# Kernel tuning notes

Measured on AMD Instinct MI355X. Metric: run time of the kernel, lower is better.

## Reference

```python
import jax, jax.numpy as jnp
import numpy as np

N = 4096      # num_nodes (tokens)
D = 1024      # in_features
GC1 = 1024    # gc hidden sizes
GC2 = 1024
FC1 = 512     # fc hidden
NUM_CLASSES = 2
FW = 8        # forward band width
BW = 8        # backward band width


def setup_inputs() -> dict:
    key = jax.random.key(0)
    ks = jax.random.split(key, 6)
    s = 0.02
    return {
        "x": jax.random.normal(ks[0], (N, D), jnp.float32),
        # sequential band weights, initialized to 0.5 as in the module
        "fw_w": 0.5 * jnp.ones((FW,), jnp.float32),
        "bw_w": 0.5 * jnp.ones((BW,), jnp.float32),
        # graph-conv layer weights (linear: h @ W + b, then A @ .)
        "gc_w1": s * jax.random.normal(ks[1], (D, GC1), jnp.float32),
        "gc_b1": jnp.zeros((GC1,), jnp.float32),
        "gc_w2": s * jax.random.normal(ks[2], (GC1, GC2), jnp.float32),
        "gc_b2": jnp.zeros((GC2,), jnp.float32),
        # fully-connected head
        "fc_w1": s * jax.random.normal(ks[3], (GC2, FC1), jnp.float32),
        "fc_b1": jnp.zeros((FC1,), jnp.float32),
        "fc_w2": s * jax.random.normal(ks[4], (FC1, NUM_CLASSES), jnp.float32),
        "fc_b2": jnp.zeros((NUM_CLASSES,), jnp.float32),
    }


def build_adjacency(fw_w, bw_w, n):
    # banded adjacency: self-loops + forward superdiagonals + backward subdiagonals,
    # then symmetric normalization D^{-1/2} A D^{-1/2}
    a = jnp.eye(n, dtype=fw_w.dtype)
    for j in range(fw_w.shape[0]):          # small fixed band loop (FW)
        a = a + fw_w[j] * jnp.eye(n, k=j + 1, dtype=fw_w.dtype)
    for j in range(bw_w.shape[0]):          # small fixed band loop (BW)
        a = a + bw_w[j] * jnp.eye(n, k=-(j + 1), dtype=bw_w.dtype)
    d = a.sum(axis=1) ** -0.5               # row degrees
    return d[:, None] * a * d[None, :]


def reference(x, fw_w, bw_w, gc_w1, gc_b1, gc_w2, gc_b2, fc_w1, fc_b1, fc_w2, fc_b2):
    a = build_adjacency(fw_w, bw_w, x.shape[0])          # [N, N]
    # GC layers: selu(A @ (H W + b)); dropout=0.0 -> identity
    h = jax.nn.selu(a @ (x @ gc_w1 + gc_b1))             # [N, GC1]
    h = jax.nn.selu(a @ (h @ gc_w2 + gc_b2))             # [N, GC2]
    pooled = h.mean(axis=0)                              # mean pooling over nodes
    z = jax.nn.selu(pooled @ fc_w1 + fc_b1)              # [FC1]
    return z @ fc_w2 + fc_b2                             # [NUM_CLASSES] logits
```

## Files before the change

kernel.cpp:

```cpp
#include <hip/hip_runtime.h>
#include <stdint.h>

#define NND 4096
#define DIM 1024
#define FC1N 512

typedef __attribute__((ext_vector_type(8))) short short8;
typedef __attribute__((ext_vector_type(4))) float floatx4;
typedef unsigned short u16;
typedef unsigned int u32;

__device__ __forceinline__ u16 f2bf(float f) {
    union { float f; u32 u; } a; a.f = f;
    u32 u = a.u;
    return (u16)((u + 0x7fffu + ((u >> 16) & 1u)) >> 16);
}
__device__ __forceinline__ float bf2f(u16 h) {
    union { u32 u; float f; } a; a.u = ((u32)h) << 16; return a.f;
}
__device__ __forceinline__ float selu_f(float x) {
    const float lam = 1.0507009873554805f;
    const float alp = 1.6732632423543772f;
    return x > 0.f ? lam * x : lam * alp * (expf(x) - 1.f);
}
__device__ __forceinline__ void async16(const u16* g, u16* l) {
    __builtin_amdgcn_global_load_lds((const __attribute__((address_space(1))) u32*)g,
                                     (__attribute__((address_space(3))) u32*)l, 16, 0, 0);
}

__global__ void k_prep(const float* __restrict__ x, const float* __restrict__ w1,
                       const float* __restrict__ w2, u16* __restrict__ Xb,
                       u16* __restrict__ W1t, u16* __restrict__ W2t,
                       float* __restrict__ zero_base) {
    int b = blockIdx.x, t = threadIdx.x;
    if (b < 512) {
        const float4* xin = (const float4*)x;
        ushort4* xo = (ushort4*)Xb;
        int base = b * 2048 + t;
        #pragma unroll
        for (int i = 0; i < 8; ++i) {
            float4 v = xin[base + i * 256];
            ushort4 o; o.x = f2bf(v.x); o.y = f2bf(v.y); o.z = f2bf(v.z); o.w = f2bf(v.w);
            xo[base + i * 256] = o;
        }
        if (b == 0)
            for (int i = t; i < 1537; i += 256) zero_base[i] = 0.f;
        return;
    }
    int job = b - 512;
    const float* in = (job & 256) ? w2 : w1;
    u16* out = (job & 256) ? W2t : W1t;
    int tl = job & 255;
    int r0 = (tl >> 4) * 64, c0 = (tl & 15) * 64;
    __shared__ float tile[64][65];
    int cg = t & 15, rb = t >> 4;
    #pragma unroll
    for (int rr = 0; rr < 4; ++rr) {
        int row = rb + rr * 16;
        float4 v = *(const float4*)(in + (size_t)(r0 + row) * DIM + c0 + cg * 4);
        tile[row][cg * 4 + 0] = v.x; tile[row][cg * 4 + 1] = v.y;
        tile[row][cg * 4 + 2] = v.z; tile[row][cg * 4 + 3] = v.w;
    }
    __syncthreads();
    #pragma unroll
    for (int rr = 0; rr < 4; ++rr) {
        int nl = rb + rr * 16;
        int kl = cg * 4;
        ushort4 o;
        o.x = f2bf(tile[kl + 0][nl]); o.y = f2bf(tile[kl + 1][nl]);
        o.z = f2bf(tile[kl + 2][nl]); o.w = f2bf(tile[kl + 3][nl]);
        *(ushort4*)(out + (size_t)(c0 + nl) * DIM + r0 + kl) = o;
    }
}

__launch_bounds__(256, 4)
__global__ void k_gemmband(const u16* __restrict__ A, const u16* __restrict__ Bt,
                           const float* __restrict__ bias,
                           const float* __restrict__ fw, const float* __restrict__ bw,
                           u16* __restrict__ H, float* __restrict__ pooled, int mode) {
    __shared__ __align__(16) u16 stage[10240];
    __shared__ float sdinv_s[96];
    __shared__ float wt_s[17];
    __shared__ float pl[4][64];

    const int m0 = blockIdx.x * 64, n0 = blockIdx.y * 64;
    const int t = threadIdx.x, wave = t >> 6, lane = t & 63;
    const int q = lane >> 4, r = lane & 15;
    const int wm = wave & 1, wn = wave >> 1;
    const int Lrow = lane >> 3, Lseg = lane & 7;

    if (t < 96) {
        int g = m0 - 16 + t;
        float s = 0.f;
        if (g >= 0 && g < NND) {
            float deg = 1.f;
            #pragma unroll
            for (int j = 0; j < 8; ++j) {
                if (g + j + 1 < NND) deg += fw[j];
                if (g - j - 1 >= 0)  deg += bw[j];
            }
            s = 1.f / sqrtf(deg);
        }
        sdinv_s[t] = s;
    } else if (t >= 128 && t < 145) {
        int o = t - 136;
        wt_s[t - 128] = (o == 0) ? 1.f : (o > 0 ? fw[o - 1] : bw[-o - 1]);
    }

    floatx4 acc[3][2];
    #pragma unroll
    for (int mt = 0; mt < 3; ++mt) { acc[mt][0] = (floatx4)0.f; acc[mt][1] = (floatx4)0.f; }

    #pragma unroll 1
    for (int k = 0; k < 16; ++k) {
        int kb = k * 64;
        #pragma unroll
        for (int i = 0; i < 5; ++i) {
            int c = wave * 5 + i;
            u16* dst = &stage[c * 512];
            const u16* src;
            if (c < 12) {
                int row = c * 8 + Lrow;
                int g = m0 - 16 + row;
                g = g < 0 ? 0 : (g > NND - 1 ? NND - 1 : g);
                src = A + (size_t)g * DIM + kb + ((Lseg ^ Lrow) * 8);
            } else {
                int row = (c - 12) * 8 + Lrow;
                src = Bt + (size_t)(n0 + row) * DIM + kb + ((Lseg ^ Lrow) * 8);
            }
            async16(src, dst);
        }
        __syncthreads();
        const u16* As = &stage[0];
        const u16* Bs = &stage[6144];
        #pragma unroll
        for (int s = 0; s < 2; ++s) {
            int j0 = s * 4 + q;
            short8 bfr[2];
            #pragma unroll
            for (int nt = 0; nt < 2; ++nt) {
                int nl = wn * 32 + nt * 16 + r;
                bfr[nt] = *(const short8*)&Bs[nl * 64 + ((j0 ^ (nl & 7)) * 8)];
            }
            #pragma unroll
            for (int mt = 0; mt < 3; ++mt) {
                int ml = wm * 48 + mt * 16 + r;
                short8 afr = *(const short8*)&As[ml * 64 + ((j0 ^ (ml & 7)) * 8)];
                acc[mt][0] = __builtin_amdgcn_mfma_f32_16x16x32_bf16(afr, bfr[0], acc[mt][0], 0, 0, 0);
                acc[mt][1] = __builtin_amdgcn_mfma_f32_16x16x32_bf16(afr, bfr[1], acc[mt][1], 0, 0, 0);
            }
        }
        __syncthreads();
    }
    u16 (*Yt)[66] = (u16(*)[66])&stage[0];
    #pragma unroll
    for (int nt = 0; nt < 2; ++nt) {
        int col = wn * 32 + nt * 16 + r;
        float bv = bias[n0 + col];
        #pragma unroll
        for (int mt = 0; mt < 3; ++mt)
            #pragma unroll
            for (int rr = 0; rr < 4; ++rr)
                Yt[wm * 48 + mt * 16 + q * 4 + rr][col] = f2bf(acc[mt][nt][rr] + bv);
    }
    __syncthreads();

    int col = t & 63;
    int r0w = (t >> 6) * 16;
    float w[17];
    #pragma unroll
    for (int o = 0; o < 17; ++o) w[o] = wt_s[o];
    float win[17];
    #pragma unroll
    for (int j = 0; j < 16; ++j) {
        int T = r0w + 8 + j;
        win[j] = sdinv_s[T] * bf2f(Yt[T][col]);
    }
    float psum = 0.f;
    #pragma unroll
    for (int rr = 0; rr < 16; ++rr) {
        int T = r0w + 24 + rr;
        win[(rr + 16) % 17] = sdinv_s[T] * bf2f(Yt[T][col]);
        float a = 0.f;
        #pragma unroll
        for (int o = 0; o < 17; ++o) a += w[o] * win[(rr + o) % 17];
        float v = selu_f(a * sdinv_s[r0w + 16 + rr]);
        if (mode == 0) H[(size_t)(m0 + r0w + rr) * DIM + n0 + col] = f2bf(v);
        else psum += v;
    }
    if (mode) {
        pl[wave][col] = psum;
        __syncthreads();
        if (t < 64)
            atomicAdd(&pooled[n0 + t], pl[0][t] + pl[1][t] + pl[2][t] + pl[3][t]);
    }
}

__global__ void k_fc(const float* __restrict__ pooled, const float* __restrict__ fcw1,
                     const float* __restrict__ fcb1, const float* __restrict__ fcw2,
                     const float* __restrict__ fcb2, float* __restrict__ zacc,
                     u32* __restrict__ cnt, float* __restrict__ out) {
    __shared__ float red[1024];
    __shared__ int lastf;
    int o = threadIdx.x, b = blockIdx.x;
    int kb = b * 64;
    float s = 0.f;
    #pragma unroll 4
    for (int kk = 0; kk < 64; ++kk)
        s += pooled[kb + kk] * fcw1[(size_t)(kb + kk) * FC1N + o];
    atomicAdd(&zacc[o], s * (1.f / NND));
    __threadfence();
    __syncthreads();
    if (o == 0) lastf = (atomicAdd(cnt, 1u) == 15u);
    __syncthreads();
    if (!lastf) return;
    __threadfence();
    float zv = atomicAdd(&zacc[o], 0.f);
    float z = selu_f(zv + fcb1[o]);
    red[o] = z * fcw2[o * 2 + 0];
    red[512 + o] = z * fcw2[o * 2 + 1];
    __syncthreads();
    #pragma unroll 1
    for (int s2 = 256; s2 > 0; s2 >>= 1) {
        if (o < s2) { red[o] += red[o + s2]; red[512 + o] += red[512 + o + s2]; }
        __syncthreads();
    }
    if (o == 0) { out[0] = red[0] + fcb2[0]; out[1] = red[1] + fcb2[1]; }
}

extern "C" void kernel_launch(void* const* d_in, const int* in_sizes, int n_in,
                              void* d_out, int out_size, void* d_ws, size_t ws_size,
                              hipStream_t stream) {
    const float* x     = (const float*)d_in[0];
    const float* fw    = (const float*)d_in[1];
    const float* bw    = (const float*)d_in[2];
    const float* gc_w1 = (const float*)d_in[3];
    const float* gc_b1 = (const float*)d_in[4];
    const float* gc_w2 = (const float*)d_in[5];
    const float* gc_b2 = (const float*)d_in[6];
    const float* fc_w1 = (const float*)d_in[7];
    const float* fc_b1 = (const float*)d_in[8];
    const float* fc_w2 = (const float*)d_in[9];
    const float* fc_b2 = (const float*)d_in[10];
    float* out = (float*)d_out;

    char* ws = (char*)d_ws;
    u16*   Xb     = (u16*)(ws);
    u16*   H1     = (u16*)(ws + (8u  << 20));
    u16*   W1t    = (u16*)(ws + (16u << 20));
    u16*   W2t    = (u16*)(ws + (18u << 20));
    float* pooled = (float*)(ws + (20u << 20));
    float* zacc   = pooled + 1024;
    u32*   cnt    = (u32*)(zacc + 512);

    k_prep<<<1024, 256, 0, stream>>>(x, gc_w1, gc_w2, Xb, W1t, W2t, pooled);
    k_gemmband<<<dim3(64, 16), 256, 0, stream>>>(Xb, W1t, gc_b1, fw, bw, H1, nullptr, 0);
    k_gemmband<<<dim3(64, 16), 256, 0, stream>>>(H1, W2t, gc_b2, fw, bw, nullptr, pooled, 1);
    k_fc<<<16, 512, 0, stream>>>(pooled, fc_w1, fc_b1, fc_w2, fc_b2, zacc, cnt, out);
}
```

Measured before the change: 145.8 us.

## Apply band adjacency before GEMM and use larger double-buffered GEMM tiles

The banded normalized adjacency is now applied to the input before each linear layer (A(XW+b) = (AX)W + rowsum(A)·b). The x band is fused into the prep conversion, and a separate band kernel runs between the two GEMMs. This removes the 16-row halo recompute and the LDS transpose epilogue from the GEMM, which now uses 128x128 tiles with double-buffered async LDS loads and adds a precomputed row-sum vector for the bias term. The cost is an extra kernel launch and an extra bf16 round trip of H1 through memory, plus lower occupancy from launch bounds of 1 and larger LDS use.

```diff
diff --git a/kernel.cpp b/kernel.cpp
--- a/kernel.cpp
+++ b/kernel.cpp
@@ -27,27 +27,83 @@
     __builtin_amdgcn_global_load_lds((const __attribute__((address_space(1))) u32*)g,
                                      (__attribute__((address_space(3))) u32*)l, 16, 0, 0);
 }
+__device__ __forceinline__ float dinv_row(int i, const float* fw, const float* bw) {
+    if (i < 0 || i >= NND) return 0.f;
+    float deg = 1.f;
+    #pragma unroll
+    for (int j = 0; j < 8; ++j) {
+        if (i + j + 1 < NND) deg += fw[j];
+        if (i - j - 1 >= 0)  deg += bw[j];
+    }
+    return 1.f / sqrtf(deg);
+}
 
 __global__ void k_prep(const float* __restrict__ x, const float* __restrict__ w1,
-                       const float* __restrict__ w2, u16* __restrict__ Xb,
+                       const float* __restrict__ w2, const float* __restrict__ fw,
+                       const float* __restrict__ bw, u16* __restrict__ XA,
                        u16* __restrict__ W1t, u16* __restrict__ W2t,
-                       float* __restrict__ zero_base) {
+                       float* __restrict__ fzone) {
     int b = blockIdx.x, t = threadIdx.x;
-    if (b < 512) {
-        const float4* xin = (const float4*)x;
-        ushort4* xo = (ushort4*)Xb;
-        int base = b * 2048 + t;
-        #pragma unroll
-        for (int i = 0; i < 8; ++i) {
-            float4 v = xin[base + i * 256];
-            ushort4 o; o.x = f2bf(v.x); o.y = f2bf(v.y); o.z = f2bf(v.z); o.w = f2bf(v.w);
-            xo[base + i * 256] = o;
-        }
-        if (b == 0)
-            for (int i = t; i < 1537; i += 256) zero_base[i] = 0.f;
+    if (b < 256) {
+        __shared__ float sdv[48];
+        __shared__ float wts[17];
+        int m0 = b * 16;
+        if (t < 48) sdv[t] = dinv_row(m0 - 16 + t, fw, bw);
+        else if (t >= 64 && t < 81) {
+            int o = t - 72;
+            wts[t - 64] = (o == 0) ? 1.f : (o > 0 ? fw[o - 1] : bw[-o - 1]);
+        }
+        __syncthreads();
+        const float4* X4 = (const float4*)x;
+        ushort4* O4 = (ushort4*)XA;
+        float4 win[17];
+        #pragma unroll
+        for (int j = 0; j < 16; ++j) {
+            int g = m0 - 8 + j;
+            int gc = g < 0 ? 0 : g;
+            float s = sdv[8 + j];
+            float4 v = X4[(size_t)gc * 256 + t];
+            win[j].x = v.x * s; win[j].y = v.y * s; win[j].z = v.z * s; win[j].w = v.w * s;
+        }
+        #pragma unroll
+        for (int rr = 0; rr < 16; ++rr) {
+            int g = m0 + 8 + rr;
+            int gc = g > NND - 1 ? NND - 1 : g;
+            float s = sdv[24 + rr];
+            float4 v = X4[(size_t)gc * 256 + t];
+            int wi = (rr + 16) % 17;
+            win[wi].x = v.x * s; win[wi].y = v.y * s; win[wi].z = v.z * s; win[wi].w = v.w * s;
+            float ax = 0.f, ay = 0.f, az = 0.f, aw = 0.f;
+            #pragma unroll
+            for (int o = 0; o < 17; ++o) {
+                float w = wts[o];
+                const float4& u = win[(rr + o) % 17];
+                ax += w * u.x; ay += w * u.y; az += w * u.z; aw += w * u.w;
+            }
+            float so = sdv[16 + rr];
+            ushort4 ov;
+            ov.x = f2bf(ax * so); ov.y = f2bf(ay * so);
+            ov.z = f2bf(az * so); ov.w = f2bf(aw * so);
+            O4[(size_t)(m0 + rr) * 256 + t] = ov;
+        }
         return;
     }
-    int job = b - 512;
+    if (b == 768) {
+        float* rs = fzone + 2048;
+        for (int it = 0; it < 16; ++it) {
+            int i = it * 256 + t;
+            float di = dinv_row(i, fw, bw);
+            float s = di;
+            #pragma unroll
+            for (int kk = 1; kk <= 8; ++kk)
+                s += fw[kk - 1] * dinv_row(i + kk, fw, bw)
+                   + bw[kk - 1] * dinv_row(i - kk, fw, bw);
+            rs[i] = di * s;
+        }
+        for (int i = t; i < 1537; i += 256) fzone[i] = 0.f;
+        return;
+    }
+    int job = b - 256;
     const float* in = (job & 256) ? w2 : w1;
     u16* out = (job & 256) ? W2t : W1t;
     int tl = job & 255;
@@ -73,126 +129,150 @@
     }
 }
 
-__launch_bounds__(256, 4)
-__global__ void k_gemmband(const u16* __restrict__ A, const u16* __restrict__ Bt,
-                           const float* __restrict__ bias,
-                           const float* __restrict__ fw, const float* __restrict__ bw,
-                           u16* __restrict__ H, float* __restrict__ pooled, int mode) {
-    __shared__ __align__(16) u16 stage[10240];
-    __shared__ float sdinv_s[96];
-    __shared__ float wt_s[17];
-    __shared__ float pl[4][64];
-
-    const int m0 = blockIdx.x * 64, n0 = blockIdx.y * 64;
+__global__ void k_band(const u16* __restrict__ in, u16* __restrict__ outp,
+                       const float* __restrict__ fw, const float* __restrict__ bw) {
+    __shared__ float sdv[48];
+    __shared__ float wts[17];
+    int b = blockIdx.x, t = threadIdx.x;
+    int m0 = b * 16;
+    if (t < 48) sdv[t] = dinv_row(m0 - 16 + t, fw, bw);
+    else if (t >= 64 && t < 81) {
+        int o = t - 72;
+        wts[t - 64] = (o == 0) ? 1.f : (o > 0 ? fw[o - 1] : bw[-o - 1]);
+    }
+    __syncthreads();
+    const ushort4* I4 = (const ushort4*)in;
+    ushort4* O4 = (ushort4*)outp;
+    float4 win[17];
+    #pragma unroll
+    for (int j = 0; j < 16; ++j) {
+        int g = m0 - 8 + j;
+        int gc = g < 0 ? 0 : g;
+        float s = sdv[8 + j];
+        ushort4 v = I4[(size_t)gc * 256 + t];
+        win[j].x = bf2f(v.x) * s; win[j].y = bf2f(v.y) * s;
+        win[j].z = bf2f(v.z) * s; win[j].w = bf2f(v.w) * s;
+    }
+    #pragma unroll
+    for (int rr = 0; rr < 16; ++rr) {
+        int g = m0 + 8 + rr;
+        int gc = g > NND - 1 ? NND - 1 : g;
+        float s = sdv[24 + rr];
+        ushort4 v = I4[(size_t)gc * 256 + t];
+        int wi = (rr + 16) % 17;
+        win[wi].x = bf2f(v.x) * s; win[wi].y = bf2f(v.y) * s;
+        win[wi].z = bf2f(v.z) * s; win[wi].w = bf2f(v.w) * s;
+        float ax = 0.f, ay = 0.f, az = 0.f, aw = 0.f;
+        #pragma unroll
+        for (int o = 0; o < 17; ++o) {
+            float w = wts[o];
+            const float4& u = win[(rr + o) % 17];
+            ax += w * u.x; ay += w * u.y; az += w * u.z; aw += w * u.w;
+        }
+        float so = sdv[16 + rr];
+        ushort4 ov;
+        ov.x = f2bf(ax * so); ov.y = f2bf(ay * so);
+        ov.z = f2bf(az * so); ov.w = f2bf(aw * so);
+        O4[(size_t)(m0 + rr) * 256 + t] = ov;
+    }
+}
+
+__launch_bounds__(256, 1)
+__global__ void k_gemm(const u16* __restrict__ A, const u16* __restrict__ Bt,
+                       const float* __restrict__ bias, const float* __restrict__ rs,
+                       u16* __restrict__ H, float* __restrict__ pooled, int mode) {
+    __shared__ __align__(16) u16 stage[2][16384];
+    const int m0 = blockIdx.x * 128, n0 = blockIdx.y * 128;
     const int t = threadIdx.x, wave = t >> 6, lane = t & 63;
     const int q = lane >> 4, r = lane & 15;
     const int wm = wave & 1, wn = wave >> 1;
     const int Lrow = lane >> 3, Lseg = lane & 7;
 
-    if (t < 96) {
-        int g = m0 - 16 + t;
-        float s = 0.f;
-        if (g >= 0 && g < NND) {
-            float deg = 1.f;
-            #pragma unroll
-            for (int j = 0; j < 8; ++j) {
-                if (g + j + 1 < NND) deg += fw[j];
-                if (g - j - 1 >= 0)  deg += bw[j];
-            }
-            s = 1.f / sqrtf(deg);
-        }
-        sdinv_s[t] = s;
-    } else if (t >= 128 && t < 145) {
-        int o = t - 136;
-        wt_s[t - 128] = (o == 0) ? 1.f : (o > 0 ? fw[o - 1] : bw[-o - 1]);
-    }
-
-    floatx4 acc[3][2];
-    #pragma unroll
-    for (int mt = 0; mt < 3; ++mt) { acc[mt][0] = (floatx4)0.f; acc[mt][1] = (floatx4)0.f; }
+    floatx4 acc[4][4];
+    #pragma unroll
+    for (int i = 0; i < 4; ++i)
+        #pragma unroll
+        for (int j = 0; j < 4; ++j) acc[i][j] = (floatx4)0.f;
+
+    #pragma unroll
+    for (int i = 0; i < 8; ++i) {
+        int c = wave * 8 + i;
+        u16* dst = &stage[0][c * 512];
+        const u16* src = (c < 16)
+            ? A  + (size_t)(m0 + c * 8 + Lrow) * DIM + ((Lseg ^ Lrow) * 8)
+            : Bt + (size_t)(n0 + (c - 16) * 8 + Lrow) * DIM + ((Lseg ^ Lrow) * 8);
+        async16(src, dst);
+    }
 
     #pragma unroll 1
     for (int k = 0; k < 16; ++k) {
-        int kb = k * 64;
-        #pragma unroll
-        for (int i = 0; i < 5; ++i) {
-            int c = wave * 5 + i;
-            u16* dst = &stage[c * 512];
-            const u16* src;
-            if (c < 12) {
-                int row = c * 8 + Lrow;
-                int g = m0 - 16 + row;
-                g = g < 0 ? 0 : (g > NND - 1 ? NND - 1 : g);
-                src = A + (size_t)g * DIM + kb + ((Lseg ^ Lrow) * 8);
-            } else {
-                int row = (c - 12) * 8 + Lrow;
-                src = Bt + (size_t)(n0 + row) * DIM + kb + ((Lseg ^ Lrow) * 8);
-            }
-            async16(src, dst);
-        }
+        int cur = k & 1;
         __syncthreads();
-        const u16* As = &stage[0];
-        const u16* Bs = &stage[6144];
+        if (k < 15) {
+            int kb = (k + 1) * 64;
+            #pragma unroll
+            for (int i = 0; i < 8; ++i) {
+                int c = wave * 8 + i;
+                u16* dst = &stage[cur ^ 1][c * 512];
+                const u16* src = (c < 16)
+                    ? A  + (size_t)(m0 + c * 8 + Lrow) * DIM + kb + ((Lseg ^ Lrow) * 8)
+                    : Bt + (size_t)(n0 + (c - 16) * 8 + Lrow) * DIM + kb + ((Lseg ^ Lrow) * 8);
+                async16(src, dst);
+            }
+        }
+        const u16* As = &stage[cur][0];
+        const u16* Bs = &stage[cur][8192];
         #pragma unroll
         for (int s = 0; s < 2; ++s) {
             int j0 = s * 4 + q;
-            short8 bfr[2];
-            #pragma unroll
-            for (int nt = 0; nt < 2; ++nt) {
-                int nl = wn * 32 + nt * 16 + r;
+            short8 bfr[4];
+            #pragma unroll
+            for (int nt = 0; nt < 4; ++nt) {
+                int nl = wn * 64 + nt * 16 + r;
                 bfr[nt] = *(const short8*)&Bs[nl * 64 + ((j0 ^ (nl & 7)) * 8)];
             }
             #pragma unroll
-            for (int mt = 0; mt < 3; ++mt) {
-                int ml = wm * 48 + mt * 16 + r;
+            for (int mt = 0; mt < 4; ++mt) {
+                int ml = wm * 64 + mt * 16 + r;
                 short8 afr = *(const short8*)&As[ml * 64 + ((j0 ^ (ml & 7)) * 8)];
-                acc[mt][0] = __builtin_amdgcn_mfma_f32_16x16x32_bf16(afr, bfr[0], acc[mt][0], 0, 0, 0);
-                acc[mt][1] = __builtin_amdgcn_mfma_f32_16x16x32_bf16(afr, bfr[1], acc[mt][1], 0, 0, 0);
-            }
-        }
+                #pragma unroll
+                for (int nt = 0; nt < 4; ++nt)
+                    acc[mt][nt] = __builtin_amdgcn_mfma_f32_16x16x32_bf16(afr, bfr[nt], acc[mt][nt], 0, 0, 0);
+            }
+        }
+    }
+
+    float psum[4] = {0.f, 0.f, 0.f, 0.f};
+    float bv[4];
+    #pragma unroll
+    for (int nt = 0; nt < 4; ++nt) bv[nt] = bias[n0 + wn * 64 + nt * 16 + r];
+    #pragma unroll
+    for (int mt = 0; mt < 4; ++mt) {
+        #pragma unroll
+        for (int rr = 0; rr < 4; ++rr) {
+            int m = m0 + wm * 64 + mt * 16 + q * 4 + rr;
+            float rsm = rs[m];
+            #pragma unroll
+            for (int nt = 0; nt < 4; ++nt) {
+                float v = selu_f(acc[mt][nt][rr] + rsm * bv[nt]);
+                if (mode == 0)
+                    H[(size_t)m * DIM + n0 + wn * 64 + nt * 16 + r] = f2bf(v);
+                else psum[nt] += v;
+            }
+        }
+    }
+    if (mode) {
+        float* PL = (float*)&stage[0][0];
+        #pragma unroll
+        for (int nt = 0; nt < 4; ++nt)
+            PL[(wn * 64 + nt * 16 + r) * 8 + wm * 4 + q] = psum[nt];
         __syncthreads();
-    }
-    u16 (*Yt)[66] = (u16(*)[66])&stage[0];
-    #pragma unroll
-    for (int nt = 0; nt < 2; ++nt) {
-        int col = wn * 32 + nt * 16 + r;
-        float bv = bias[n0 + col];
-        #pragma unroll
-        for (int mt = 0; mt < 3; ++mt)
-            #pragma unroll
-            for (int rr = 0; rr < 4; ++rr)
-                Yt[wm * 48 + mt * 16 + q * 4 + rr][col] = f2bf(acc[mt][nt][rr] + bv);
-    }
-    __syncthreads();
-
-    int col = t & 63;
-    int r0w = (t >> 6) * 16;
-    float w[17];
-    #pragma unroll
-    for (int o = 0; o < 17; ++o) w[o] = wt_s[o];
-    float win[17];
-    #pragma unroll
-    for (int j = 0; j < 16; ++j) {
-        int T = r0w + 8 + j;
-        win[j] = sdinv_s[T] * bf2f(Yt[T][col]);
-    }
-    float psum = 0.f;
-    #pragma unroll
-    for (int rr = 0; rr < 16; ++rr) {
-        int T = r0w + 24 + rr;
-        win[(rr + 16) % 17] = sdinv_s[T] * bf2f(Yt[T][col]);
-        float a = 0.f;
-        #pragma unroll
-        for (int o = 0; o < 17; ++o) a += w[o] * win[(rr + o) % 17];
-        float v = selu_f(a * sdinv_s[r0w + 16 + rr]);
-        if (mode == 0) H[(size_t)(m0 + r0w + rr) * DIM + n0 + col] = f2bf(v);
-        else psum += v;
-    }
-    if (mode) {
-        pl[wave][col] = psum;
-        __syncthreads();
-        if (t < 64)
-            atomicAdd(&pooled[n0 + t], pl[0][t] + pl[1][t] + pl[2][t] + pl[3][t]);
+        if (t < 128) {
+            float s = 0.f;
+            #pragma unroll
+            for (int i = 0; i < 8; ++i) s += PL[t * 8 + i];
+            atomicAdd(&pooled[n0 + t], s);
+        }
     }
 }
 
@@ -245,16 +325,20 @@
     float* out = (float*)d_out;
 
     char* ws = (char*)d_ws;
-    u16*   Xb     = (u16*)(ws);
+    u16*   XA     = (u16*)(ws);
     u16*   H1     = (u16*)(ws + (8u  << 20));
-    u16*   W1t    = (u16*)(ws + (16u << 20));
-    u16*   W2t    = (u16*)(ws + (18u << 20));
-    float* pooled = (float*)(ws + (20u << 20));
-    float* zacc   = pooled + 1024;
-    u32*   cnt    = (u32*)(zacc + 512);
-
-    k_prep<<<1024, 256, 0, stream>>>(x, gc_w1, gc_w2, Xb, W1t, W2t, pooled);
-    k_gemmband<<<dim3(64, 16), 256, 0, stream>>>(Xb, W1t, gc_b1, fw, bw, H1, nullptr, 0);
-    k_gemmband<<<dim3(64, 16), 256, 0, stream>>>(H1, W2t, gc_b2, fw, bw, nullptr, pooled, 1);
+    u16*   H1A    = (u16*)(ws + (16u << 20));
+    u16*   W1t    = (u16*)(ws + (24u << 20));
+    u16*   W2t    = (u16*)(ws + (26u << 20));
+    float* fzone  = (float*)(ws + (28u << 20));
+    float* pooled = fzone;
+    float* zacc   = fzone + 1024;
+    u32*   cnt    = (u32*)(fzone + 1536);
+    float* rs     = fzone + 2048;
+
+    k_prep<<<769, 256, 0, stream>>>(x, gc_w1, gc_w2, fw, bw, XA, W1t, W2t, fzone);
+    k_gemm<<<dim3(32, 8), 256, 0, stream>>>(XA, W1t, gc_b1, rs, H1, nullptr, 0);
+    k_band<<<256, 256, 0, stream>>>(H1, H1A, fw, bw);
+    k_gemm<<<dim3(32, 8), 256, 0, stream>>>(H1A, W2t, gc_b2, rs, nullptr, pooled, 1);
     k_fc<<<16, 512, 0, stream>>>(pooled, fc_w1, fc_b1, fc_w2, fc_b2, zacc, cnt, out);
 }
```

New measurement: 324.3 us. +122.4%, slower.
